# Performance work log

Hardware: AMD Instinct MI355X
Metric: run time of the kernel (lower is better)

## Reference

```python
import jax, jax.numpy as jnp
import numpy as np

N, D, M = 2048, 1024, 1024


def setup_inputs() -> dict:
    key = jax.random.key(0)
    ks = jax.random.split(key, 10)
    inputs = jax.random.normal(ks[0], (N, D), jnp.float32)
    # topological parent pointers: parent[t] > t; root (t=N-1) points to dummy slot N
    p = jax.random.randint(ks[1], (N,), jnp.arange(1, N + 1), N + 1)
    parent = jnp.where(jnp.arange(N) < N - 1, jnp.minimum(p, N - 1), N)
    s = 0.02
    Wioux = jax.random.normal(ks[2], (3 * M, D), jnp.float32) * s
    bioux = jax.random.normal(ks[3], (3 * M,), jnp.float32) * s
    Wiouh = jax.random.normal(ks[4], (3 * M, M), jnp.float32) * s
    biouh = jax.random.normal(ks[5], (3 * M,), jnp.float32) * s
    Wfx = jax.random.normal(ks[6], (M, D), jnp.float32) * s
    bfx = jax.random.normal(ks[7], (M,), jnp.float32) * s
    Wfh = jax.random.normal(ks[8], (M, M), jnp.float32) * s
    bfh = jax.random.normal(ks[9], (M,), jnp.float32) * s
    return dict(inputs=inputs, parent=parent, Wioux=Wioux, bioux=bioux,
                Wiouh=Wiouh, biouh=biouh, Wfx=Wfx, bfx=bfx, Wfh=Wfh, bfh=bfh)


def reference(inputs, parent, Wioux, bioux, Wiouh, biouh, Wfx, bfx, Wfh, bfh):
    # Child-Sum Tree-LSTM over nodes in topological order (children before parents).
    n, m = inputs.shape[0], Wfx.shape[0]
    ioux_all = inputs @ Wioux.T + bioux              # [N, 3M] self.ioux(inputs) for all nodes
    fx_all = inputs @ Wfx.T + bfx                    # [N, M]  self.fx(inputs) for all nodes
    fx_pad = jnp.concatenate([fx_all, jnp.zeros((1, m), fx_all.dtype)], axis=0)
    fxp = fx_pad[parent]                             # [N, M]  fx of each node's parent

    def step(carry, xs):
        h_sum, fc_sum = carry                        # [N+1, M] accumulated child sums
        t, iou_x, fxp_t, p = xs
        iou = iou_x + h_sum[t] @ Wiouh.T + biouh     # ioux(x) + iouh(child_h_sum)
        i, o, u = jnp.split(iou, 3)
        i, o, u = jax.nn.sigmoid(i), jax.nn.sigmoid(o), jnp.tanh(u)
        c = i * u + fc_sum[t]                        # i*u + sum_k f_k * c_k
        h = o * jnp.tanh(c)
        # forget gate for this node as a child of its parent: sigmoid(fh(h) + fx(x_parent))
        f = jax.nn.sigmoid(h @ Wfh.T + bfh + fxp_t)
        return (h_sum.at[p].add(h), fc_sum.at[p].add(f * c)), (c, h)

    init = (jnp.zeros((n + 1, m), inputs.dtype), jnp.zeros((n + 1, m), inputs.dtype))
    _, (cs, hs) = jax.lax.scan(step, init,
                               (jnp.arange(n), ioux_all, fxp, parent))
    # root is the last node in topological order; torch returns (c, h) each [1, mem_dim]
    return cs[-1:], hs[-1:]
```

## Files before the change

### kernel.cpp

```cpp
#include <hip/hip_runtime.h>

#define NN 2048
#define MD 1024
#define NOUT 4096
#define GBLK 256
#define GTHR 512
#define CAP 1024

typedef __attribute__((ext_vector_type(8))) short short8;
typedef __attribute__((ext_vector_type(4))) float f4;

__device__ __forceinline__ unsigned short f2bf(float f) {
  unsigned u = __float_as_uint(f);
  u += 0x7fffu + ((u >> 16) & 1u);
  return (unsigned short)(u >> 16);
}
__device__ __forceinline__ uint4 pack8(f4 a, f4 b) {
  uint4 r;
  r.x = f2bf(a[0]) | ((unsigned)f2bf(a[1]) << 16);
  r.y = f2bf(a[2]) | ((unsigned)f2bf(a[3]) << 16);
  r.z = f2bf(b[0]) | ((unsigned)f2bf(b[1]) << 16);
  r.w = f2bf(b[2]) | ((unsigned)f2bf(b[3]) << 16);
  return r;
}
__device__ __forceinline__ float blo(unsigned u) { return __uint_as_float(u << 16); }
__device__ __forceinline__ float bhi(unsigned u) { return __uint_as_float(u & 0xffff0000u); }
__device__ __forceinline__ float sigm(float x) { return 1.0f / (1.0f + __expf(-x)); }
__device__ __forceinline__ float tanh_(float x) { return 1.0f - 2.0f / (1.0f + __expf(2.0f * x)); }

__global__ __launch_bounds__(256) void cvt_bf16_kernel(const float* __restrict__ s,
                                                       unsigned short* __restrict__ d, int n4) {
  int i = blockIdx.x * 256 + threadIdx.x;
  if (i < n4) {
    f4 v = *((const f4*)s + i);
    unsigned lo = f2bf(v[0]) | ((unsigned)f2bf(v[1]) << 16);
    unsigned hi = f2bf(v[2]) | ((unsigned)f2bf(v[3]) << 16);
    uint2 r; r.x = lo; r.y = hi;
    *((uint2*)d + i) = r;
  }
}

__global__ __launch_bounds__(1024) void prep_kernel(const int* __restrict__ parent,
                                                    int2* __restrict__ meta,
                                                    int* __restrict__ doff_g,
                                                    int* __restrict__ maxd_out,
                                                    int* __restrict__ flags,
                                                    const float* __restrict__ bioux,
                                                    const float* __restrict__ biouh,
                                                    const float* __restrict__ bfx,
                                                    const float* __restrict__ bfh,
                                                    float* __restrict__ biasC) {
  __shared__ int s_anc[NN], s_dep[NN];
  __shared__ int s_t1[NN + 2], s_t2[NN + 2];
  __shared__ int s_poff[NN + 2], s_cur[NN + 2];
  __shared__ int s_ordp[NN], s_nord[NN];
  __shared__ int s_doff[NN + 2];
  __shared__ int s_sc[NN], s_sc2[NN];
  __shared__ int s_wsum[17];
  __shared__ int s_maxd;
  const int tid = threadIdx.x;

  if (tid == 0) s_maxd = 0;
  for (int i = tid; i < GBLK + 64; i += 1024) flags[i] = 0;
  for (int i = tid; i < NOUT; i += 1024)
    biasC[i] = (i < 3072) ? (bioux[i] + biouh[i]) : (bfx[i - 3072] + bfh[i - 3072]);
  for (int t = tid; t < NN; t += 1024) {
    bool root = (t == NN - 1);
    s_anc[t] = root ? t : parent[t];
    s_dep[t] = root ? 0 : 1;
  }
  __syncthreads();
  for (int it = 0; it < 11; ++it) {
    for (int t = tid; t < NN; t += 1024) { int a = s_anc[t]; s_t1[t] = s_dep[t] + s_dep[a]; s_t2[t] = s_anc[a]; }
    __syncthreads();
    for (int t = tid; t < NN; t += 1024) { s_dep[t] = s_t1[t]; s_anc[t] = s_t2[t]; }
    __syncthreads();
  }
  for (int t = tid; t < NN; t += 1024) atomicMax(&s_maxd, s_dep[t]);

  for (int i = tid; i < NN + 2; i += 1024) s_t2[i] = 0;
  __syncthreads();
  for (int t = tid; t < NN; t += 1024) atomicAdd(&s_t2[parent[t]], 1);
  __syncthreads();
  {
    const int L = NN + 2;
    int* src = s_t2; int* dst = s_t1;
    for (int o = 1; o < L; o <<= 1) {
      for (int i = tid; i < L; i += 1024) dst[i] = src[i] + ((i >= o) ? src[i - o] : 0);
      __syncthreads();
      int* tmp = src; src = dst; dst = tmp;
    }
    for (int i = tid; i < L; i += 1024) { int v = (i ? src[i - 1] : 0); s_poff[i] = v; s_cur[i] = v; }
    __syncthreads();
    for (int t = tid; t < NN; t += 1024) {
      int pos = atomicAdd(&s_cur[parent[t]], 1);
      s_ordp[pos] = t;
    }
    __syncthreads();
    for (int p = tid; p < NN + 1; p += 1024) {
      int b = s_poff[p], e = s_poff[p + 1];
      for (int i = b + 1; i < e; ++i) {
        int v = s_ordp[i], j = i - 1;
        while (j >= b && s_ordp[j] > v) { s_ordp[j + 1] = s_ordp[j]; --j; }
        s_ordp[j + 1] = v;
      }
    }
    __syncthreads();
  }

  for (int i = tid; i < NN + 2; i += 1024) s_t2[i] = 0;
  __syncthreads();
  for (int t = tid; t < NN; t += 1024) atomicAdd(&s_t2[s_dep[t]], 1);
  __syncthreads();
  {
    const int L = NN + 1;
    int* src = s_t2; int* dst = s_t1;
    for (int o = 1; o < L; o <<= 1) {
      for (int i = tid; i < L; i += 1024) dst[i] = src[i] + ((i >= o) ? src[i - o] : 0);
      __syncthreads();
      int* tmp = src; src = dst; dst = tmp;
    }
    for (int i = tid; i < L + 1; i += 1024) s_doff[i] = (i ? src[i - 1] : 0);
    __syncthreads();
  }

  const int maxd = s_maxd;
  if (tid == 0) s_nord[0] = NN - 1;
  __syncthreads();
  for (int d = 0; d < maxd; ++d) {
    const int lbeg = s_doff[d], lend = s_doff[d + 1];
    const int nd = lend - lbeg;
    if (nd <= 1024) {
      int t = -1, v = 0;
      if (tid < nd) { t = s_nord[lbeg + tid]; v = s_poff[t + 1] - s_poff[t]; }
      #pragma unroll
      for (int o = 1; o < 64; o <<= 1) {
        int u = __shfl_up(v, (unsigned)o, 64);
        if ((tid & 63) >= o) v += u;
      }
      if ((tid & 63) == 63) s_wsum[tid >> 6] = v;
      __syncthreads();
      if (tid < 16) {
        int w = s_wsum[tid];
        #pragma unroll
        for (int o = 1; o < 16; o <<= 1) {
          int u = __shfl_up(w, (unsigned)o, 16);
          if (tid >= o) w += u;
        }
        s_wsum[tid] = w;
      }
      __syncthreads();
      if (tid < nd) {
        int incl = v + ((tid >> 6) ? s_wsum[(tid >> 6) - 1] : 0);
        int cnti = s_poff[t + 1] - s_poff[t];
        int crel = incl - cnti;
        meta[lbeg + tid] = make_int2(t, (crel << 16) | cnti);
        for (int j = 0; j < cnti; ++j) s_nord[lend + crel + j] = s_ordp[s_poff[t] + j];
      }
      __syncthreads();
    } else {
      for (int i = tid; i < nd; i += 1024) { int t2 = s_nord[lbeg + i]; s_sc[i] = s_poff[t2 + 1] - s_poff[t2]; }
      __syncthreads();
      for (int o = 1; o < nd; o <<= 1) {
        for (int i = tid; i < nd; i += 1024) s_sc2[i] = s_sc[i] + ((i >= o) ? s_sc[i - o] : 0);
        __syncthreads();
        for (int i = tid; i < nd; i += 1024) s_sc[i] = s_sc2[i];
        __syncthreads();
      }
      for (int i = tid; i < nd; i += 1024) {
        int t2 = s_nord[lbeg + i];
        int cnti = s_poff[t2 + 1] - s_poff[t2];
        int crel = s_sc[i] - cnti;
        meta[lbeg + i] = make_int2(t2, (crel << 16) | cnti);
        for (int j = 0; j < cnti; ++j) s_nord[lend + crel + j] = s_ordp[s_poff[t2] + j];
      }
      __syncthreads();
    }
  }
  {
    const int lbeg = s_doff[maxd], lend = s_doff[maxd + 1];
    for (int i = lbeg + tid; i < lend; i += 1024)
      meta[i] = make_int2(s_nord[i], 0);
  }
  for (int i = tid; i <= maxd + 1; i += 1024) doff_g[i] = s_doff[i];
  if (tid == 0) *maxd_out = maxd;
}

__global__ __launch_bounds__(256) void pregemm_kernel(const unsigned short* __restrict__ Xb,
                                                      const float* __restrict__ Wioux,
                                                      const float* __restrict__ Wfx,
                                                      unsigned short* __restrict__ XWb,
                                                      const float* __restrict__ biasC) {
  __shared__ alignas(16) unsigned short ldsA[64 * 40];
  __shared__ alignas(16) unsigned short ldsB[64 * 40];
  const int xcd = blockIdx.x & 7;
  const int w = blockIdx.x >> 3;
  const int tn = xcd * 8 + (w & 7);
  const int tm = w >> 3;
  const int m0 = tm * 64, n0 = tn * 64;
  const int tid = threadIdx.x;
  const int lane = tid & 63;
  const int wave = tid >> 6;
  const int wr = wave >> 1, wc = wave & 1;
  f4 acc[2][2] = {};
  const int sr = tid >> 2;
  const int sc = (tid & 3) << 3;
  const unsigned short* agp = Xb + (size_t)(m0 + sr) * MD + sc;
  const int brow = n0 + sr;
  const float* bgp = (brow < 3072) ? (Wioux + (size_t)brow * MD + sc)
                                   : (Wfx + (size_t)(brow - 3072) * MD + sc);
  const int lr = lane & 15;
  const int kq = (lane >> 4) << 3;

  for (int k0 = 0; k0 < MD; k0 += 32) {
    uint4 av = *(const uint4*)(agp + k0);
    f4 blo_ = *(const f4*)(bgp + k0);
    f4 bhi_ = *(const f4*)(bgp + k0 + 4);
    __syncthreads();
    *(uint4*)&ldsA[sr * 40 + sc] = av;
    *(uint4*)&ldsB[sr * 40 + sc] = pack8(blo_, bhi_);
    __syncthreads();
    short8 a0 = *(const short8*)&ldsA[(wr * 32 + lr) * 40 + kq];
    short8 a1 = *(const short8*)&ldsA[(wr * 32 + 16 + lr) * 40 + kq];
    short8 b0 = *(const short8*)&ldsB[(wc * 32 + lr) * 40 + kq];
    short8 b1 = *(const short8*)&ldsB[(wc * 32 + 16 + lr) * 40 + kq];
    acc[0][0] = __builtin_amdgcn_mfma_f32_16x16x32_bf16(a0, b0, acc[0][0], 0, 0, 0);
    acc[0][1] = __builtin_amdgcn_mfma_f32_16x16x32_bf16(a0, b1, acc[0][1], 0, 0, 0);
    acc[1][0] = __builtin_amdgcn_mfma_f32_16x16x32_bf16(a1, b0, acc[1][0], 0, 0, 0);
    acc[1][1] = __builtin_amdgcn_mfma_f32_16x16x32_bf16(a1, b1, acc[1][1], 0, 0, 0);
  }
  for (int r = 0; r < 2; ++r)
    for (int c = 0; c < 2; ++c)
      for (int q = 0; q < 4; ++q) {
        const int row = m0 + wr * 32 + r * 16 + (lane >> 4) * 4 + q;
        const int col = n0 + wc * 32 + c * 16 + lr;
        const float v = acc[r][c][q] + biasC[col];
        const int g = col >> 10, cj = col & 1023;
        XWb[((size_t)(cj >> 2) * NN + row) * 16 + (g << 2) + (cj & 3)] = f2bf(v);
      }
}

struct RP {
  const int2* meta;
  const int* doff;
  const int* maxd;
  const unsigned short* XWb;
  unsigned short* G2;
  float* CbB;
  unsigned short* Hb;
  const float* Wiouh;
  const float* Wfh;
  float* out;
  int* flags;
};

__device__ __forceinline__ void grid_barrier(int* flags, int step) {
  asm volatile("s_waitcnt vmcnt(0)" ::: "memory");
  __syncthreads();
  int* epoch = flags + GBLK;
  if (blockIdx.x == 0) {
    if (threadIdx.x < 64) {
      if (threadIdx.x == 0)
        __hip_atomic_store(&flags[0], step, __ATOMIC_RELAXED, __HIP_MEMORY_SCOPE_AGENT);
      const int base = threadIdx.x << 2;
      for (;;) {
        int a = __hip_atomic_load(&flags[base + 0], __ATOMIC_RELAXED, __HIP_MEMORY_SCOPE_AGENT);
        int b = __hip_atomic_load(&flags[base + 1], __ATOMIC_RELAXED, __HIP_MEMORY_SCOPE_AGENT);
        int c = __hip_atomic_load(&flags[base + 2], __ATOMIC_RELAXED, __HIP_MEMORY_SCOPE_AGENT);
        int d = __hip_atomic_load(&flags[base + 3], __ATOMIC_RELAXED, __HIP_MEMORY_SCOPE_AGENT);
        if (__all(a >= step && b >= step && c >= step && d >= step)) break;
        __builtin_amdgcn_s_sleep(1);
      }
      if (threadIdx.x == 0)
        __hip_atomic_store(epoch, step, __ATOMIC_RELAXED, __HIP_MEMORY_SCOPE_AGENT);
    }
  } else if (threadIdx.x == 0) {
    __hip_atomic_store(&flags[blockIdx.x], step, __ATOMIC_RELAXED, __HIP_MEMORY_SCOPE_AGENT);
    while (__hip_atomic_load(epoch, __ATOMIC_RELAXED, __HIP_MEMORY_SCOPE_AGENT) < step)
      __builtin_amdgcn_s_sleep(1);
  }
  __syncthreads();
  asm volatile("" ::: "memory");
}

#define GSTEP(A, KB)                                                                     \
  {                                                                                      \
    short8 bfrag = *(const short8*)(wb0 + ((((KB << 2) + kq) ^ swz) << 3));              \
    if ((KB) & 1) ao = __builtin_amdgcn_mfma_f32_16x16x32_bf16(A, bfrag, ao, 0, 0, 0);   \
    else          ae = __builtin_amdgcn_mfma_f32_16x16x32_bf16(A, bfrag, ae, 0, 0, 0);   \
    if ((KB) + 16 < 32) A = *(const short8*)(ap + (((KB) + 16) << 5));                   \
  }

__global__ __launch_bounds__(GTHR) void recur_kernel(RP p) {
  __shared__ alignas(16) unsigned short ldsW[16 * MD];
  __shared__ alignas(16) unsigned short G2L[CAP * 16];
  __shared__ alignas(16) float CbL[2 * CAP * 4];
  __shared__ int2 ldsMeta[NN];
  __shared__ int ldsDoff[NN + 2];
  const int tid = threadIdx.x;
  const int bid = blockIdx.x;
  const int lane = tid & 63;
  const int wave = tid >> 6;
  const int strip = (bid & 7) * 32 + (bid >> 3);
  const int s4 = strip << 2;

  for (int idx = tid; idx < 16 * 128; idx += GTHR) {
    int j = idx >> 7, kc = idx & 127;
    int g = j >> 2, col = s4 + (j & 3);
    const float* src = (g < 3) ? (p.Wiouh + (size_t)(g * MD + col) * MD)
                               : (p.Wfh + (size_t)col * MD);
    f4 lo = *(const f4*)(src + (kc << 3));
    f4 hi = *(const f4*)(src + (kc << 3) + 4);
    *(uint4*)(ldsW + j * MD + ((kc ^ (j & 7)) << 3)) = pack8(lo, hi);
  }
  const int maxd = *p.maxd;
  for (int i = tid; i < NN; i += GTHR) ldsMeta[i] = p.meta[i];
  for (int i = tid; i <= maxd + 1; i += GTHR) ldsDoff[i] = p.doff[i];
  __syncthreads();

  const unsigned short* xwb = p.XWb + (size_t)strip * NN * 16;
  unsigned short* G2g = p.G2 + (size_t)bid * NN * 16;
  float* CbBg = p.CbB + (size_t)bid * NN * 4;
  const int chalf = tid & 1;

  for (int d = maxd; d >= 0; --d) {
    const int lbeg = ldsDoff[d], lend = ldsDoff[d + 1];
    const int nd = lend - lbeg;
    float* cbw = CbL + (size_t)(d & 1) * CAP * 4;
    const float* cbr = CbL + (size_t)((d + 1) & 1) * CAP * 4;

    for (int ii = tid >> 1; ii < nd; ii += GTHR / 2) {
      const int2 mt = ldsMeta[lbeg + ii];
      const int t = mt.x, crel = mt.y >> 16, cnt = mt.y & 0xffff;
      const unsigned short* xwp = xwb + (size_t)t * 16;
      uint4 xa = *(const uint4*)xwp;
      uint4 xb = *(const uint4*)(xwp + 8);
      f4 gf; gf[0] = blo(xb.z); gf[1] = bhi(xb.z); gf[2] = blo(xb.w); gf[3] = bhi(xb.w);
      f4 gi = {0.f, 0.f, 0.f, 0.f}, go = gi, gu = gi, fc = gi;
      if (chalf == 0) {
        gi[0] = blo(xa.x); gi[1] = bhi(xa.x); gi[2] = blo(xa.y); gi[3] = bhi(xa.y);
        go[0] = blo(xa.z); go[1] = bhi(xa.z); go[2] = blo(xa.w); go[3] = bhi(xa.w);
        gu[0] = blo(xb.x); gu[1] = bhi(xb.x); gu[2] = blo(xb.y); gu[3] = bhi(xb.y);
      }
      for (int k = chalf; k < cnt; k += 2) {
        const int ci = crel + k;
        uint4 ga, gb; f4 cu;
        if (ci < CAP) {
          ga = *(const uint4*)(G2L + ci * 16);
          gb = *(const uint4*)(G2L + ci * 16 + 8);
          cu = *(const f4*)(cbr + ci * 4);
        } else {
          const unsigned short* g2 = G2g + (size_t)(lend + ci) * 16;
          ga = *(const uint4*)(g2);
          gb = *(const uint4*)(g2 + 8);
          cu = *(const f4*)(CbBg + (size_t)(lend + ci) * 4);
        }
        gi[0] += blo(ga.x); gi[1] += bhi(ga.x); gi[2] += blo(ga.y); gi[3] += bhi(ga.y);
        go[0] += blo(ga.z); go[1] += bhi(ga.z); go[2] += blo(ga.w); go[3] += bhi(ga.w);
        gu[0] += blo(gb.x); gu[1] += bhi(gb.x); gu[2] += blo(gb.y); gu[3] += bhi(gb.y);
        f4 gff; gff[0] = blo(gb.z); gff[1] = bhi(gb.z); gff[2] = blo(gb.w); gff[3] = bhi(gb.w);
        #pragma unroll
        for (int q = 0; q < 4; ++q) fc[q] += sigm(gff[q] + gf[q]) * cu[q];
      }
      #pragma unroll
      for (int q = 0; q < 4; ++q) {
        gi[q] += __shfl_xor(gi[q], 1);
        go[q] += __shfl_xor(go[q], 1);
        gu[q] += __shfl_xor(gu[q], 1);
        fc[q] += __shfl_xor(fc[q], 1);
      }
      if (chalf == 0) {
        f4 cv, hv;
        #pragma unroll
        for (int q = 0; q < 4; ++q) {
          float c0 = sigm(gi[q]) * tanh_(gu[q]) + fc[q];
          cv[q] = c0;
          hv[q] = sigm(go[q]) * tanh_(c0);
        }
        if (ii < CAP) *(f4*)(cbw + ii * 4) = cv;
        else          *(f4*)(CbBg + (size_t)(lbeg + ii) * 4) = cv;
        unsigned long long hp =
            (unsigned long long)f2bf(hv[0]) |
            ((unsigned long long)f2bf(hv[1]) << 16) |
            ((unsigned long long)f2bf(hv[2]) << 32) |
            ((unsigned long long)f2bf(hv[3]) << 48);
        __hip_atomic_store((unsigned long long*)(p.Hb + (size_t)t * MD + s4),
                           hp, __ATOMIC_RELAXED, __HIP_MEMORY_SCOPE_AGENT);
        if (t == NN - 1) {
          *(f4*)(p.out + s4) = cv;
          *(f4*)(p.out + MD + s4) = hv;
        }
      }
    }
    if (d == 0) break;

    grid_barrier(p.flags, maxd - d + 1);

    if (d > 0) {
      const int lbeg2 = ldsDoff[d - 1];
      const int nd2 = lbeg - lbeg2;
      for (int q2 = tid; q2 < nd2; q2 += GTHR) {
        unsigned v = *(const unsigned*)(xwb + (size_t)ldsMeta[lbeg2 + q2].x * 16);
        asm volatile("" :: "v"(v));
      }
    }

    {
      const int ntr = (nd + 15) >> 4;
      const int lr = lane & 15;
      const int kq = lane >> 4;
      const int swz = lr & 7;
      const unsigned short* wb0 = ldsW + lr * MD;
      for (int rt = wave; rt < ntr; rt += GTHR / 64) {
        const int r = (rt << 4) + lr;
        const int pos = lbeg + ((r < nd) ? r : 0);
        const int node = ldsMeta[pos].x;
        const unsigned short* ap = p.Hb + (size_t)node * MD + (kq << 3);
        short8 A0  = *(const short8*)(ap);
        short8 A1  = *(const short8*)(ap + 32);
        short8 A2  = *(const short8*)(ap + 64);
        short8 A3  = *(const short8*)(ap + 96);
        short8 A4  = *(const short8*)(ap + 128);
        short8 A5  = *(const short8*)(ap + 160);
        short8 A6  = *(const short8*)(ap + 192);
        short8 A7  = *(const short8*)(ap + 224);
        short8 A8  = *(const short8*)(ap + 256);
        short8 A9  = *(const short8*)(ap + 288);
        short8 A10 = *(const short8*)(ap + 320);
        short8 A11 = *(const short8*)(ap + 352);
        short8 A12 = *(const short8*)(ap + 384);
        short8 A13 = *(const short8*)(ap + 416);
        short8 A14 = *(const short8*)(ap + 448);
        short8 A15 = *(const short8*)(ap + 480);
        f4 ae = {0.f, 0.f, 0.f, 0.f}, ao = {0.f, 0.f, 0.f, 0.f};
        GSTEP(A0, 0)   GSTEP(A1, 1)   GSTEP(A2, 2)   GSTEP(A3, 3)
        GSTEP(A4, 4)   GSTEP(A5, 5)   GSTEP(A6, 6)   GSTEP(A7, 7)
        GSTEP(A8, 8)   GSTEP(A9, 9)   GSTEP(A10, 10) GSTEP(A11, 11)
        GSTEP(A12, 12) GSTEP(A13, 13) GSTEP(A14, 14) GSTEP(A15, 15)
        GSTEP(A0, 16)  GSTEP(A1, 17)  GSTEP(A2, 18)  GSTEP(A3, 19)
        GSTEP(A4, 20)  GSTEP(A5, 21)  GSTEP(A6, 22)  GSTEP(A7, 23)
        GSTEP(A8, 24)  GSTEP(A9, 25)  GSTEP(A10, 26) GSTEP(A11, 27)
        GSTEP(A12, 28) GSTEP(A13, 29) GSTEP(A14, 30) GSTEP(A15, 31)
        const int rb = (rt << 4) + (kq << 2);
        #pragma unroll
        for (int q = 0; q < 4; ++q) {
          const int rr = rb + q;
          if (rr < nd) {
            unsigned short v = f2bf(ae[q] + ao[q]);
            if (rr < CAP) G2L[rr * 16 + lr] = v;
            else          G2g[(size_t)(lbeg + rr) * 16 + lr] = v;
          }
        }
      }
    }
    __syncthreads();
  }
}

extern "C" void kernel_launch(void* const* d_in, const int* in_sizes, int n_in,
                              void* d_out, int out_size, void* d_ws, size_t ws_size,
                              hipStream_t stream) {
  const float* X     = (const float*)d_in[0];
  const int*   parent= (const int*)d_in[1];
  const float* Wioux = (const float*)d_in[2];
  const float* bioux = (const float*)d_in[3];
  const float* Wiouh = (const float*)d_in[4];
  const float* biouh = (const float*)d_in[5];
  const float* Wfx   = (const float*)d_in[6];
  const float* bfx   = (const float*)d_in[7];
  const float* Wfh   = (const float*)d_in[8];
  const float* bfh   = (const float*)d_in[9];
  float* out = (float*)d_out;

  char* ws = (char*)d_ws;
  size_t o = 0;
  auto alloc = [&](size_t bytes) { size_t r = o; o += (bytes + 255) & ~(size_t)255; return r; };
  unsigned short* Xb   = (unsigned short*)(ws + alloc((size_t)NN * MD * 2));
  unsigned short* XWb  = (unsigned short*)(ws + alloc((size_t)GBLK * NN * 16 * 2));
  unsigned short* G2   = (unsigned short*)(ws + alloc((size_t)GBLK * NN * 16 * 2));
  float* CbB           = (float*)(ws + alloc((size_t)GBLK * NN * 4 * 4));
  unsigned short* Hb   = (unsigned short*)(ws + alloc((size_t)NN * MD * 2));
  float* biasC         = (float*)(ws + alloc((size_t)NOUT * 4));
  int2* meta           = (int2*)(ws + alloc((size_t)NN * 8));
  int* doff            = (int*)(ws + alloc((NN + 4) * 4));
  int* maxd            = (int*)(ws + alloc(256));
  int* flags           = (int*)(ws + alloc((GBLK + 64) * 4));

  cvt_bf16_kernel<<<(NN * MD / 4 + 255) / 256, 256, 0, stream>>>(X, Xb, NN * MD / 4);

  prep_kernel<<<1, 1024, 0, stream>>>(parent, meta, doff, maxd, flags,
                                      bioux, biouh, bfx, bfh, biasC);

  pregemm_kernel<<<(NN / 64) * (NOUT / 64), 256, 0, stream>>>(Xb, Wioux, Wfx, XWb, biasC);

  RP p;
  p.meta = meta; p.doff = doff; p.maxd = maxd;
  p.XWb = XWb; p.G2 = G2; p.CbB = CbB; p.Hb = Hb;
  p.Wiouh = Wiouh; p.Wfh = Wfh;
  p.out = out; p.flags = flags;
  void* args[] = {&p};
  hipLaunchCooperativeKernel((const void*)recur_kernel, dim3(GBLK), dim3(GTHR), args, 0, stream);

  (void)in_sizes; (void)n_in; (void)out_size; (void)ws_size;
}
```

Measured before the change: 347.7 us.

## Pre-convert weights to bf16 and use 128x128 tiles with direct global-to-LDS loads

The conversion kernel now also converts Wioux and Wfx to bf16 into a packed weight buffer, so the input-projection GEMM no longer converts fp32 weights inside its k-loop. The GEMM tile grows from 64x64 to 128x128, with each wave computing a 4x4 grid of MFMA tiles, and operands are staged through global_load_lds builtins. This targets the GEMM's per-tile conversion and load overhead and raises compute per loaded byte. In exchange it adds an extra 8MB bf16 weight write, uses unpadded LDS rows that may bank-conflict, and launches only 512 blocks, which means fewer waves in flight.

```diff
diff --git a/kernel.cpp b/kernel.cpp
--- a/kernel.cpp
+++ b/kernel.cpp
@@ -28,16 +28,25 @@
 __device__ __forceinline__ float sigm(float x) { return 1.0f / (1.0f + __expf(-x)); }
 __device__ __forceinline__ float tanh_(float x) { return 1.0f - 2.0f / (1.0f + __expf(2.0f * x)); }
 
-__global__ __launch_bounds__(256) void cvt_bf16_kernel(const float* __restrict__ s,
-                                                       unsigned short* __restrict__ d, int n4) {
+__global__ __launch_bounds__(256) void cvt_all_kernel(const float* __restrict__ X,
+                                                      const float* __restrict__ Wioux,
+                                                      const float* __restrict__ Wfx,
+                                                      unsigned short* __restrict__ Xb,
+                                                      unsigned short* __restrict__ Wpre) {
+  const int nX = NN * MD / 4;
+  const int nWi = 3072 * MD / 4;
+  const int nWf = 1024 * MD / 4;
   int i = blockIdx.x * 256 + threadIdx.x;
-  if (i < n4) {
-    f4 v = *((const f4*)s + i);
-    unsigned lo = f2bf(v[0]) | ((unsigned)f2bf(v[1]) << 16);
-    unsigned hi = f2bf(v[2]) | ((unsigned)f2bf(v[3]) << 16);
-    uint2 r; r.x = lo; r.y = hi;
-    *((uint2*)d + i) = r;
-  }
+  const float* s; unsigned short* d; int off;
+  if (i < nX) { s = X; d = Xb; off = i; }
+  else if (i < nX + nWi) { s = Wioux; d = Wpre; off = i - nX; }
+  else if (i < nX + nWi + nWf) { s = Wfx; d = Wpre + (size_t)3072 * MD; off = i - nX - nWi; }
+  else return;
+  f4 v = *((const f4*)s + off);
+  uint2 r;
+  r.x = f2bf(v[0]) | ((unsigned)f2bf(v[1]) << 16);
+  r.y = f2bf(v[2]) | ((unsigned)f2bf(v[3]) << 16);
+  *((uint2*)d + off) = r;
 }
 
 __global__ __launch_bounds__(1024) void prep_kernel(const int* __restrict__ parent,
@@ -187,54 +196,62 @@
 }
 
 __global__ __launch_bounds__(256) void pregemm_kernel(const unsigned short* __restrict__ Xb,
-                                                      const float* __restrict__ Wioux,
-                                                      const float* __restrict__ Wfx,
+                                                      const unsigned short* __restrict__ Wpre,
                                                       unsigned short* __restrict__ XWb,
                                                       const float* __restrict__ biasC) {
-  __shared__ alignas(16) unsigned short ldsA[64 * 40];
-  __shared__ alignas(16) unsigned short ldsB[64 * 40];
+  __shared__ alignas(16) unsigned short ldsA[128 * 32];
+  __shared__ alignas(16) unsigned short ldsB[128 * 32];
   const int xcd = blockIdx.x & 7;
   const int w = blockIdx.x >> 3;
-  const int tn = xcd * 8 + (w & 7);
-  const int tm = w >> 3;
-  const int m0 = tm * 64, n0 = tn * 64;
+  const int tn = xcd * 4 + (w & 3);
+  const int tm = w >> 2;
+  const int m0 = tm * 128, n0 = tn * 128;
   const int tid = threadIdx.x;
   const int lane = tid & 63;
   const int wave = tid >> 6;
   const int wr = wave >> 1, wc = wave & 1;
-  f4 acc[2][2] = {};
-  const int sr = tid >> 2;
-  const int sc = (tid & 3) << 3;
-  const unsigned short* agp = Xb + (size_t)(m0 + sr) * MD + sc;
-  const int brow = n0 + sr;
-  const float* bgp = (brow < 3072) ? (Wioux + (size_t)brow * MD + sc)
-                                   : (Wfx + (size_t)(brow - 3072) * MD + sc);
   const int lr = lane & 15;
-  const int kq = (lane >> 4) << 3;
+  const int kq = lane >> 4;
+  const int srow = lane >> 2;
+  const int scol = (lane & 3) << 3;
+  f4 acc[4][4] = {};
 
   for (int k0 = 0; k0 < MD; k0 += 32) {
-    uint4 av = *(const uint4*)(agp + k0);
-    f4 blo_ = *(const f4*)(bgp + k0);
-    f4 bhi_ = *(const f4*)(bgp + k0 + 4);
-    __syncthreads();
-    *(uint4*)&ldsA[sr * 40 + sc] = av;
-    *(uint4*)&ldsB[sr * 40 + sc] = pack8(blo_, bhi_);
-    __syncthreads();
-    short8 a0 = *(const short8*)&ldsA[(wr * 32 + lr) * 40 + kq];
-    short8 a1 = *(const short8*)&ldsA[(wr * 32 + 16 + lr) * 40 + kq];
-    short8 b0 = *(const short8*)&ldsB[(wc * 32 + lr) * 40 + kq];
-    short8 b1 = *(const short8*)&ldsB[(wc * 32 + 16 + lr) * 40 + kq];
-    acc[0][0] = __builtin_amdgcn_mfma_f32_16x16x32_bf16(a0, b0, acc[0][0], 0, 0, 0);
-    acc[0][1] = __builtin_amdgcn_mfma_f32_16x16x32_bf16(a0, b1, acc[0][1], 0, 0, 0);
-    acc[1][0] = __builtin_amdgcn_mfma_f32_16x16x32_bf16(a1, b0, acc[1][0], 0, 0, 0);
-    acc[1][1] = __builtin_amdgcn_mfma_f32_16x16x32_bf16(a1, b1, acc[1][1], 0, 0, 0);
-  }
-  for (int r = 0; r < 2; ++r)
-    for (int c = 0; c < 2; ++c)
+    #pragma unroll
+    for (int c = 0; c < 2; ++c) {
+      const int chunk = wave * 2 + c;
+      const unsigned short* ga = Xb + (size_t)(m0 + chunk * 16 + srow) * MD + k0 + scol;
+      const unsigned short* gb = Wpre + (size_t)(n0 + chunk * 16 + srow) * MD + k0 + scol;
+      __builtin_amdgcn_global_load_lds((const __attribute__((address_space(1))) void*)ga,
+                                       (__attribute__((address_space(3))) void*)&ldsA[chunk * 512],
+                                       16, 0, 0);
+      __builtin_amdgcn_global_load_lds((const __attribute__((address_space(1))) void*)gb,
+                                       (__attribute__((address_space(3))) void*)&ldsB[chunk * 512],
+                                       16, 0, 0);
+    }
+    __syncthreads();
+    short8 a[4], b[4];
+    #pragma unroll
+    for (int i = 0; i < 4; ++i) {
+      a[i] = *(const short8*)&ldsA[(wr * 64 + i * 16 + lr) * 32 + kq * 8];
+      b[i] = *(const short8*)&ldsB[(wc * 64 + i * 16 + lr) * 32 + kq * 8];
+    }
+    #pragma unroll
+    for (int i = 0; i < 4; ++i)
+      #pragma unroll
+      for (int j = 0; j < 4; ++j)
+        acc[i][j] = __builtin_amdgcn_mfma_f32_16x16x32_bf16(a[i], b[j], acc[i][j], 0, 0, 0);
+    __syncthreads();
+  }
+  #pragma unroll
+  for (int i = 0; i < 4; ++i)
+    #pragma unroll
+    for (int j = 0; j < 4; ++j)
+      #pragma unroll
       for (int q = 0; q < 4; ++q) {
-        const int row = m0 + wr * 32 + r * 16 + (lane >> 4) * 4 + q;
-        const int col = n0 + wc * 32 + c * 16 + lr;
-        const float v = acc[r][c][q] + biasC[col];
+        const int row = m0 + wr * 64 + i * 16 + kq * 4 + q;
+        const int col = n0 + wc * 64 + j * 16 + lr;
+        const float v = acc[i][j][q] + biasC[col];
         const int g = col >> 10, cj = col & 1023;
         XWb[((size_t)(cj >> 2) * NN + row) * 16 + (g << 2) + (cj & 3)] = f2bf(v);
       }
@@ -476,6 +493,7 @@
   size_t o = 0;
   auto alloc = [&](size_t bytes) { size_t r = o; o += (bytes + 255) & ~(size_t)255; return r; };
   unsigned short* Xb   = (unsigned short*)(ws + alloc((size_t)NN * MD * 2));
+  unsigned short* Wpre = (unsigned short*)(ws + alloc((size_t)NOUT * MD * 2));
   unsigned short* XWb  = (unsigned short*)(ws + alloc((size_t)GBLK * NN * 16 * 2));
   unsigned short* G2   = (unsigned short*)(ws + alloc((size_t)GBLK * NN * 16 * 2));
   float* CbB           = (float*)(ws + alloc((size_t)GBLK * NN * 4 * 4));
@@ -486,12 +504,15 @@
   int* maxd            = (int*)(ws + alloc(256));
   int* flags           = (int*)(ws + alloc((GBLK + 64) * 4));
 
-  cvt_bf16_kernel<<<(NN * MD / 4 + 255) / 256, 256, 0, stream>>>(X, Xb, NN * MD / 4);
+  {
+    const int n4 = (NN * MD + 3072 * MD + 1024 * MD) / 4;
+    cvt_all_kernel<<<(n4 + 255) / 256, 256, 0, stream>>>(X, Wioux, Wfx, Xb, Wpre);
+  }
 
   prep_kernel<<<1, 1024, 0, stream>>>(parent, meta, doff, maxd, flags,
                                       bioux, biouh, bfx, bfh, biasC);
 
-  pregemm_kernel<<<(NN / 64) * (NOUT / 64), 256, 0, stream>>>(Xb, Wioux, Wfx, XWb, biasC);
+  pregemm_kernel<<<(NN / 128) * (NOUT / 128), 256, 0, stream>>>(Xb, Wpre, XWb, biasC);
 
   RP p;
   p.meta = meta; p.doff = doff; p.maxd = maxd;
```

Result: faster. 336.0 us (-3.4%).
